# Kernel optimization log

Hardware: AMD Instinct MI355X
Metric: run time of the kernel (lower is better)

The kernel has to match this reference:

```python
import jax, jax.numpy as jnp
import numpy as np


def _cell_centered_coords(H, W):
    # cell-centered unit grid: coordinate k -> (k + 0.5) / n, meshgrid over (h1, w1, h2, w2)
    h = (jnp.arange(H, dtype=jnp.float32) + 0.5) / H
    w = (jnp.arange(W, dtype=jnp.float32) + 0.5) / W
    g = jnp.meshgrid(h, w, h, w, indexing='ij')
    return jnp.stack(g, axis=-1)  # (H, W, H, W, 4)


def setup_inputs() -> dict:
    key = jax.random.key(0)
    ks = jax.random.split(key, 6)
    B, I, O, H, W, HID = 8, 16, 16, 28, 28, 64
    s1 = 1.0 / np.sqrt(4.0)
    s2 = 1.0 / np.sqrt(HID)
    return {
        'v': jax.random.normal(ks[0], (B, I, H, W), dtype=jnp.float32),
        'W1': jax.random.uniform(ks[1], (4, HID), jnp.float32, -s1, s1),
        'b1': jax.random.uniform(ks[2], (HID,), jnp.float32, -s1, s1),
        'W2': jax.random.uniform(ks[3], (HID, O * I), jnp.float32, -s2, s2),
        'b2': jax.random.uniform(ks[4], (O * I,), jnp.float32, -s2, s2),
        'bias': jax.random.uniform(ks[5], (O, 1, 1), jnp.float32, -1.0 / np.sqrt(I), 1.0 / np.sqrt(I)),
    }


def reference(v, W1, b1, W2, b2, bias):
    H, W = v.shape[-2], v.shape[-1]
    I = v.shape[-3]
    O = W2.shape[-1] // I
    coords = _cell_centered_coords(H, W)                      # (H,W,H,W,4)
    hidden = jax.nn.gelu(coords @ W1 + b1, approximate=False)  # (H,W,H,W,64)
    kernel = (hidden @ W2 + b2).reshape(H, W, H, W, O, I)      # (h1,w1,h2,w2,O,I)
    # midpoint-rule quadrature weights on the unit square: 1/(H*W) per cell
    quad = 1.0 / (H * W)
    # einsum 'h1 w1 h2 w2 o i, n i h1 w2 -> n o h2 w2' (w1 summed out of kernel alone)
    out = jnp.einsum('pqrsoi,nips->nors', kernel, quad * v)
    return out + bias
```

## Files before the change

kernel.cpp:

```cpp
#include <hip/hip_runtime.h>

#define Hn 28
#define PQ 784
#define NI 128

typedef __attribute__((ext_vector_type(8))) short short8v;
typedef __attribute__((ext_vector_type(4))) short short4v;
typedef __attribute__((ext_vector_type(4))) float float4v;

__device__ __forceinline__ short f2bf(float x) {
    union { float f; unsigned u; } a; a.f = x;
    unsigned r = a.u + 0x7FFF + ((a.u >> 16) & 1);
    return (short)(r >> 16);
}

__global__ __launch_bounds__(256, 4) void fused_kernel(
    const float* __restrict__ v, const float* __restrict__ W1,
    const float* __restrict__ b1, const float* __restrict__ W2,
    const float* __restrict__ b2, const float* __restrict__ bias,
    float* __restrict__ out)
{
    __shared__ short sV[NI * 40];
    __shared__ short sHt[64 * 40];
    __shared__ short sTa[8 * 1032];
    __shared__ float sRed[4 * 256];
    __shared__ float sVs[NI];

    const int t = threadIdx.x;
    const int rs = blockIdx.x;
    const int r = rs / Hn;
    const int s = rs - r * Hn;

    const int ni0 = t & 127;
    const int p0 = t >> 7;
    float vreg[14];
    #pragma unroll
    for (int j = 0; j < 14; ++j) {
        vreg[j] = v[ni0 * PQ + (p0 + 2 * j) * Hn + s];
    }

    {
        const int c = t & 63;
        const int pg = t >> 6;
        const float w0 = W1[c];
        const float Wc = W1[64 + c];
        const float w2 = W1[128 + c];
        const float w3 = W1[192 + c];
        const float inv = 1.0f / 28.0f;
        const float base = ((r + 0.5f) * inv) * w2 + ((s + 0.5f) * inv) * w3
                         + b1[c] + 0.5f * Wc;
        const float w0i = inv * w0;
        const float W2c = Wc * Wc;
        const float c2 = 1.1651786f * W2c;
        const float c4 = 0.0145213f * (W2c * W2c);
        #pragma unroll
        for (int pi = 0; pi < 7; ++pi) {
            const int p = pg * 7 + pi;
            const float m  = fmaf((float)p + 0.5f, w0i, base);
            const float m2 = m * m;
            const float E  = __builtin_amdgcn_exp2f(m2 * -0.72134752f);
            const float az = fabsf(m) * 0.70710678f;
            const float tt = __builtin_amdgcn_rcpf(fmaf(0.3275911f, az, 1.0f));
            float poly = fmaf(tt, 1.061405429f, -1.453152027f);
            poly = fmaf(tt, poly, 1.421413741f);
            poly = fmaf(tt, poly, -0.284496736f);
            poly = fmaf(tt, poly, 0.254829592f);
            poly = poly * tt;
            float erfv = fmaf(-poly, E, 1.0f);
            erfv = (m < 0.0f) ? -erfv : erfv;
            const float g   = 0.5f * m * (1.0f + erfv);
            const float phi = 0.39894228f * E;
            const float p4  = fmaf(-m2, m2, fmaf(7.0f, m2, -4.0f));
            const float corr = phi * fmaf(c4, p4, c2 * (2.0f - m2));
            sHt[c * 40 + p] = f2bf(fmaf(28.0f, g, corr));
        }
        if (pg == 3) *(uint2*)&sHt[c * 40 + 28] = make_uint2(0u, 0u);
    }

    {
        float psum = 0.0f;
        #pragma unroll
        for (int j = 0; j < 14; ++j) {
            psum += vreg[j];
            sV[ni0 * 40 + (p0 + 2 * j)] = f2bf(vreg[j]);
        }
        sRed[t] = psum;
        if (t < NI) *(uint2*)&sV[t * 40 + 28] = make_uint2(0u, 0u);
    }
    __syncthreads();

    if (t < NI) sVs[t] = sRed[t] + sRed[t + NI];

    const int w  = t >> 6;
    const int l  = t & 63;
    const int lm = l & 15;
    const int q  = l >> 4;
    const int k0 = q * 8;

    {
        short8v aF[2], bF[4];
        aF[0] = *(const short8v*)&sV[(32 * w + lm) * 40 + k0];
        aF[1] = *(const short8v*)&sV[(32 * w + 16 + lm) * 40 + k0];
        #pragma unroll
        for (int nt = 0; nt < 4; ++nt)
            bF[nt] = *(const short8v*)&sHt[(16 * nt + lm) * 40 + k0];

        float4v accD[2][4];
        #pragma unroll
        for (int mt = 0; mt < 2; ++mt)
            #pragma unroll
            for (int nt = 0; nt < 4; ++nt)
                accD[mt][nt] = __builtin_amdgcn_mfma_f32_16x16x32_bf16(
                    aF[mt], bF[nt], (float4v)(0.0f), 0, 0, 0);

        #pragma unroll
        for (int mt = 0; mt < 2; ++mt) {
            const int n8 = 2 * w + mt;
            #pragma unroll
            for (int nt = 0; nt < 4; ++nt) {
                const int c = 16 * nt + lm;
                short4v pk;
                pk[0] = f2bf(accD[mt][nt][0]);
                pk[1] = f2bf(accD[mt][nt][1]);
                pk[2] = f2bf(accD[mt][nt][2]);
                pk[3] = f2bf(accD[mt][nt][3]);
                *(short4v*)&sTa[n8 * 1032 + c * 16 + 4 * q] = pk;
            }
        }
    }
    __syncthreads();

    float4v accO = (float4v)(0.0f);
    #pragma unroll
    for (int st = 0; st < 8; ++st) {
        const int kb = w * 256 + st * 32 + k0;
        const short8v a = *(const short8v*)&sTa[(lm & 7) * 1032 + kb];
        const int c  = kb >> 4;
        const int i0 = kb & 15;
        const float* wrow = &W2[c * 256 + lm * 16 + i0];
        const float4 wf0 = *(const float4*)&wrow[0];
        const float4 wf1 = *(const float4*)&wrow[4];
        short8v bfr;
        bfr[0] = f2bf(wf0.x); bfr[1] = f2bf(wf0.y);
        bfr[2] = f2bf(wf0.z); bfr[3] = f2bf(wf0.w);
        bfr[4] = f2bf(wf1.x); bfr[5] = f2bf(wf1.y);
        bfr[6] = f2bf(wf1.z); bfr[7] = f2bf(wf1.w);
        accO = __builtin_amdgcn_mfma_f32_16x16x32_bf16(a, bfr, accO, 0, 0, 0);
    }
    __syncthreads();
    #pragma unroll
    for (int reg = 0; reg < 4; ++reg) {
        const int m = q * 4 + reg;
        sRed[w * 256 + m * 16 + lm] = accO[reg];
    }
    __syncthreads();

    if (t < NI) {
        const int n8 = t >> 4;
        const int o  = t & 15;
        const int e  = n8 * 16 + o;
        const float tot = sRed[e] + sRed[256 + e] + sRed[512 + e] + sRed[768 + e];
        float bsum = 0.0f;
        #pragma unroll
        for (int i = 0; i < 16; ++i)
            bsum = fmaf(b2[o * 16 + i], sVs[n8 * 16 + i], bsum);
        out[(n8 * 16 + o) * PQ + rs] = (tot + 28.0f * bsum) * (1.0f / 784.0f) + bias[o];
    }
}

extern "C" void kernel_launch(void* const* d_in, const int* in_sizes, int n_in,
                              void* d_out, int out_size, void* d_ws, size_t ws_size,
                              hipStream_t stream) {
    const float* v    = (const float*)d_in[0];
    const float* W1   = (const float*)d_in[1];
    const float* b1   = (const float*)d_in[2];
    const float* W2   = (const float*)d_in[3];
    const float* b2   = (const float*)d_in[4];
    const float* bias = (const float*)d_in[5];
    float* out = (float*)d_out;

    fused_kernel<<<PQ, 256, 0, stream>>>(v, W1, b1, W2, b2, bias, out);
}
```

Measured before the change: 80.18 us.

## Process four output rows per block and cache bf16 W2 fragments in registers

Each block now loops over four r values for a fixed s, reducing the grid from 784 to 196 blocks. The W2 fragments are loaded and converted to bf16 once per block into registers, and the v tile and its sums are staged once and reused across the four iterations. This removes redundant global W2 traffic and conversions, at the cost of fewer blocks than compute units, serialized per-block work, and higher register pressure.

```diff
diff --git a/kernel.cpp b/kernel.cpp
--- a/kernel.cpp
+++ b/kernel.cpp
@@ -27,9 +27,15 @@
     __shared__ float sVs[NI];
 
     const int t = threadIdx.x;
-    const int rs = blockIdx.x;
-    const int r = rs / Hn;
-    const int s = rs - r * Hn;
+    const int b = blockIdx.x;
+    const int s = b / 7;
+    const int g = b - s * 7;
+
+    const int w  = t >> 6;
+    const int l  = t & 63;
+    const int lm = l & 15;
+    const int q  = l >> 4;
+    const int k0 = q * 8;
 
     const int ni0 = t & 127;
     const int p0 = t >> 7;
@@ -39,102 +45,10 @@
         vreg[j] = v[ni0 * PQ + (p0 + 2 * j) * Hn + s];
     }
 
-    {
-        const int c = t & 63;
-        const int pg = t >> 6;
-        const float w0 = W1[c];
-        const float Wc = W1[64 + c];
-        const float w2 = W1[128 + c];
-        const float w3 = W1[192 + c];
-        const float inv = 1.0f / 28.0f;
-        const float base = ((r + 0.5f) * inv) * w2 + ((s + 0.5f) * inv) * w3
-                         + b1[c] + 0.5f * Wc;
-        const float w0i = inv * w0;
-        const float W2c = Wc * Wc;
-        const float c2 = 1.1651786f * W2c;
-        const float c4 = 0.0145213f * (W2c * W2c);
-        #pragma unroll
-        for (int pi = 0; pi < 7; ++pi) {
-            const int p = pg * 7 + pi;
-            const float m  = fmaf((float)p + 0.5f, w0i, base);
-            const float m2 = m * m;
-            const float E  = __builtin_amdgcn_exp2f(m2 * -0.72134752f);
-            const float az = fabsf(m) * 0.70710678f;
-            const float tt = __builtin_amdgcn_rcpf(fmaf(0.3275911f, az, 1.0f));
-            float poly = fmaf(tt, 1.061405429f, -1.453152027f);
-            poly = fmaf(tt, poly, 1.421413741f);
-            poly = fmaf(tt, poly, -0.284496736f);
-            poly = fmaf(tt, poly, 0.254829592f);
-            poly = poly * tt;
-            float erfv = fmaf(-poly, E, 1.0f);
-            erfv = (m < 0.0f) ? -erfv : erfv;
-            const float g   = 0.5f * m * (1.0f + erfv);
-            const float phi = 0.39894228f * E;
-            const float p4  = fmaf(-m2, m2, fmaf(7.0f, m2, -4.0f));
-            const float corr = phi * fmaf(c4, p4, c2 * (2.0f - m2));
-            sHt[c * 40 + p] = f2bf(fmaf(28.0f, g, corr));
-        }
-        if (pg == 3) *(uint2*)&sHt[c * 40 + 28] = make_uint2(0u, 0u);
-    }
-
-    {
-        float psum = 0.0f;
-        #pragma unroll
-        for (int j = 0; j < 14; ++j) {
-            psum += vreg[j];
-            sV[ni0 * 40 + (p0 + 2 * j)] = f2bf(vreg[j]);
-        }
-        sRed[t] = psum;
-        if (t < NI) *(uint2*)&sV[t * 40 + 28] = make_uint2(0u, 0u);
-    }
-    __syncthreads();
-
-    if (t < NI) sVs[t] = sRed[t] + sRed[t + NI];
-
-    const int w  = t >> 6;
-    const int l  = t & 63;
-    const int lm = l & 15;
-    const int q  = l >> 4;
-    const int k0 = q * 8;
-
-    {
-        short8v aF[2], bF[4];
-        aF[0] = *(const short8v*)&sV[(32 * w + lm) * 40 + k0];
-        aF[1] = *(const short8v*)&sV[(32 * w + 16 + lm) * 40 + k0];
-        #pragma unroll
-        for (int nt = 0; nt < 4; ++nt)
-            bF[nt] = *(const short8v*)&sHt[(16 * nt + lm) * 40 + k0];
-
-        float4v accD[2][4];
-        #pragma unroll
-        for (int mt = 0; mt < 2; ++mt)
-            #pragma unroll
-            for (int nt = 0; nt < 4; ++nt)
-                accD[mt][nt] = __builtin_amdgcn_mfma_f32_16x16x32_bf16(
-                    aF[mt], bF[nt], (float4v)(0.0f), 0, 0, 0);
-
-        #pragma unroll
-        for (int mt = 0; mt < 2; ++mt) {
-            const int n8 = 2 * w + mt;
-            #pragma unroll
-            for (int nt = 0; nt < 4; ++nt) {
-                const int c = 16 * nt + lm;
-                short4v pk;
-                pk[0] = f2bf(accD[mt][nt][0]);
-                pk[1] = f2bf(accD[mt][nt][1]);
-                pk[2] = f2bf(accD[mt][nt][2]);
-                pk[3] = f2bf(accD[mt][nt][3]);
-                *(short4v*)&sTa[n8 * 1032 + c * 16 + 4 * q] = pk;
-            }
-        }
-    }
-    __syncthreads();
-
-    float4v accO = (float4v)(0.0f);
+    short8v wcache[8];
     #pragma unroll
     for (int st = 0; st < 8; ++st) {
         const int kb = w * 256 + st * 32 + k0;
-        const short8v a = *(const short8v*)&sTa[(lm & 7) * 1032 + kb];
         const int c  = kb >> 4;
         const int i0 = kb & 15;
         const float* wrow = &W2[c * 256 + lm * 16 + i0];
@@ -145,26 +59,126 @@
         bfr[2] = f2bf(wf0.z); bfr[3] = f2bf(wf0.w);
         bfr[4] = f2bf(wf1.x); bfr[5] = f2bf(wf1.y);
         bfr[6] = f2bf(wf1.z); bfr[7] = f2bf(wf1.w);
-        accO = __builtin_amdgcn_mfma_f32_16x16x32_bf16(a, bfr, accO, 0, 0, 0);
+        wcache[st] = bfr;
     }
-    __syncthreads();
-    #pragma unroll
-    for (int reg = 0; reg < 4; ++reg) {
-        const int m = q * 4 + reg;
-        sRed[w * 256 + m * 16 + lm] = accO[reg];
-    }
-    __syncthreads();
 
-    if (t < NI) {
-        const int n8 = t >> 4;
-        const int o  = t & 15;
-        const int e  = n8 * 16 + o;
-        const float tot = sRed[e] + sRed[256 + e] + sRed[512 + e] + sRed[768 + e];
-        float bsum = 0.0f;
+    const int c_ = t & 63;
+    const int pg = t >> 6;
+    const float w0 = W1[c_];
+    const float Wc = W1[64 + c_];
+    const float w2_ = W1[128 + c_];
+    const float w3_ = W1[192 + c_];
+    const float b1c = b1[c_];
+    const float inv = 1.0f / 28.0f;
+    const float w0i = inv * w0;
+    const float W2c = Wc * Wc;
+    const float c2 = 1.1651786f * W2c;
+    const float c4 = 0.0145213f * (W2c * W2c);
+    const float base_s = ((s + 0.5f) * inv) * w3_ + b1c + 0.5f * Wc;
+
+    #pragma unroll 1
+    for (int rr = 0; rr < 4; ++rr) {
+        const int r = 4 * g + rr;
+
+        {
+            const float base = ((r + 0.5f) * inv) * w2_ + base_s;
+            #pragma unroll
+            for (int pi = 0; pi < 7; ++pi) {
+                const int p = pg * 7 + pi;
+                const float m  = fmaf((float)p + 0.5f, w0i, base);
+                const float m2 = m * m;
+                const float E  = __builtin_amdgcn_exp2f(m2 * -0.72134752f);
+                const float az = fabsf(m) * 0.70710678f;
+                const float tt = __builtin_amdgcn_rcpf(fmaf(0.3275911f, az, 1.0f));
+                float poly = fmaf(tt, 1.061405429f, -1.453152027f);
+                poly = fmaf(tt, poly, 1.421413741f);
+                poly = fmaf(tt, poly, -0.284496736f);
+                poly = fmaf(tt, poly, 0.254829592f);
+                poly = poly * tt;
+                float erfv = fmaf(-poly, E, 1.0f);
+                erfv = (m < 0.0f) ? -erfv : erfv;
+                const float gg  = 0.5f * m * (1.0f + erfv);
+                const float phi = 0.39894228f * E;
+                const float p4  = fmaf(-m2, m2, fmaf(7.0f, m2, -4.0f));
+                const float corr = phi * fmaf(c4, p4, c2 * (2.0f - m2));
+                sHt[c_ * 40 + p] = f2bf(fmaf(28.0f, gg, corr));
+            }
+            if (pg == 3) *(uint2*)&sHt[c_ * 40 + 28] = make_uint2(0u, 0u);
+        }
+
+        if (rr == 0) {
+            float psum = 0.0f;
+            #pragma unroll
+            for (int j = 0; j < 14; ++j) {
+                psum += vreg[j];
+                sV[ni0 * 40 + (p0 + 2 * j)] = f2bf(vreg[j]);
+            }
+            sRed[t] = psum;
+            if (t < NI) *(uint2*)&sV[t * 40 + 28] = make_uint2(0u, 0u);
+        }
+        __syncthreads();
+
+        if (rr == 0 && t < NI) sVs[t] = sRed[t] + sRed[t + NI];
+
+        {
+            short8v aF[2], bF[4];
+            aF[0] = *(const short8v*)&sV[(32 * w + lm) * 40 + k0];
+            aF[1] = *(const short8v*)&sV[(32 * w + 16 + lm) * 40 + k0];
+            #pragma unroll
+            for (int nt = 0; nt < 4; ++nt)
+                bF[nt] = *(const short8v*)&sHt[(16 * nt + lm) * 40 + k0];
+
+            float4v accD[2][4];
+            #pragma unroll
+            for (int mt = 0; mt < 2; ++mt)
+                #pragma unroll
+                for (int nt = 0; nt < 4; ++nt)
+                    accD[mt][nt] = __builtin_amdgcn_mfma_f32_16x16x32_bf16(
+                        aF[mt], bF[nt], (float4v)(0.0f), 0, 0, 0);
+
+            #pragma unroll
+            for (int mt = 0; mt < 2; ++mt) {
+                const int n8 = 2 * w + mt;
+                #pragma unroll
+                for (int nt = 0; nt < 4; ++nt) {
+                    const int c = 16 * nt + lm;
+                    short4v pk;
+                    pk[0] = f2bf(accD[mt][nt][0]);
+                    pk[1] = f2bf(accD[mt][nt][1]);
+                    pk[2] = f2bf(accD[mt][nt][2]);
+                    pk[3] = f2bf(accD[mt][nt][3]);
+                    *(short4v*)&sTa[n8 * 1032 + c * 16 + 4 * q] = pk;
+                }
+            }
+        }
+        __syncthreads();
+
+        float4v accO = (float4v)(0.0f);
         #pragma unroll
-        for (int i = 0; i < 16; ++i)
-            bsum = fmaf(b2[o * 16 + i], sVs[n8 * 16 + i], bsum);
-        out[(n8 * 16 + o) * PQ + rs] = (tot + 28.0f * bsum) * (1.0f / 784.0f) + bias[o];
+        for (int st = 0; st < 8; ++st) {
+            const int kb = w * 256 + st * 32 + k0;
+            const short8v a = *(const short8v*)&sTa[(lm & 7) * 1032 + kb];
+            accO = __builtin_amdgcn_mfma_f32_16x16x32_bf16(a, wcache[st], accO, 0, 0, 0);
+        }
+        #pragma unroll
+        for (int reg = 0; reg < 4; ++reg) {
+            const int m = q * 4 + reg;
+            sRed[w * 256 + m * 16 + lm] = accO[reg];
+        }
+        __syncthreads();
+
+        if (t < NI) {
+            const int n8 = t >> 4;
+            const int o  = t & 15;
+            const int e  = n8 * 16 + o;
+            const float tot = sRed[e] + sRed[256 + e] + sRed[512 + e] + sRed[768 + e];
+            float bsum = 0.0f;
+            #pragma unroll
+            for (int i = 0; i < 16; ++i)
+                bsum = fmaf(b2[o * 16 + i], sVs[n8 * 16 + i], bsum);
+            out[(n8 * 16 + o) * PQ + r * Hn + s] =
+                (tot + 28.0f * bsum) * (1.0f / 784.0f) + bias[o];
+        }
     }
 }
 
@@ -179,5 +193,5 @@
     const float* bias = (const float*)d_in[5];
     float* out = (float*)d_out;
 
-    fused_kernel<<<PQ, 256, 0, stream>>>(v, W1, b1, W2, b2, bias, out);
+    fused_kernel<<<196, 256, 0, stream>>>(v, W1, b1, W2, b2, bias, out);
 }
```

Result: faster. 74.11 us (-7.6%).
